# Kernel optimization log

Measured on AMD Instinct MI355X. Metric: run time of the kernel, lower is better.

## Reference

```python
import jax, jax.numpy as jnp
import numpy as np

INPUT_SIZE = 128
OUTPUT_SIZE = 200000
K = 4096
MOMENTUM = 0.5
BATCH = 128


def setup_inputs() -> dict:
    key = jax.random.key(0)
    k1, k2, k3, k4, k5, k6, k7, k8 = jax.random.split(key, 8)
    stdv = 1.0 / np.sqrt(INPUT_SIZE / 3.0)
    inp = {
        "l": jax.random.normal(k1, (BATCH, INPUT_SIZE), jnp.float32),
        "ab": jax.random.normal(k2, (BATCH, INPUT_SIZE), jnp.float32),
        "ori": jax.random.normal(k3, (BATCH, INPUT_SIZE), jnp.float32),
        "y": jax.random.randint(k4, (BATCH,), 0, OUTPUT_SIZE, jnp.int32),
        "idx": jax.random.randint(k5, (BATCH, K + 1), 0, OUTPUT_SIZE, jnp.int32),
        # memory banks ~ U(-stdv, stdv), as in the torch buffer init
        "memory_l": jax.random.uniform(k6, (OUTPUT_SIZE, INPUT_SIZE), jnp.float32, -stdv, stdv),
        "memory_ab": jax.random.uniform(k7, (OUTPUT_SIZE, INPUT_SIZE), jnp.float32, -stdv, stdv),
        "memory_ori": jax.random.uniform(k8, (OUTPUT_SIZE, INPUT_SIZE), jnp.float32, -stdv, stdv),
    }
    return inp


def reference(l, ab, ori, y, idx, memory_l, memory_ab, memory_ori):
    # Gather [B, K+1, D] slices from each memory bank (detached in original).
    w_l = jax.lax.stop_gradient(memory_l[idx])
    w_ab = jax.lax.stop_gradient(memory_ab[idx])
    w_ori = jax.lax.stop_gradient(memory_ori[idx])

    # bmm((B,K+1,D), (B,D,1)) -> (B,K+1); stack 6 score tensors -> (6,B,K+1)
    out_ab2l = jnp.einsum("bkd,bd->bk", w_l, ab)
    out_l2ab = jnp.einsum("bkd,bd->bk", w_ab, l)
    out_l2ori = jnp.einsum("bkd,bd->bk", w_ori, l)
    out_ori2l = jnp.einsum("bkd,bd->bk", w_l, ori)
    out_ori2ab = jnp.einsum("bkd,bd->bk", w_ab, ori)
    out_ab2ori = jnp.einsum("bkd,bd->bk", w_ori, ab)
    outs = jnp.stack([out_ab2l, out_l2ab, out_ori2l, out_l2ori, out_ab2ori, out_ori2ab])

    # Momentum scatter update of the memory banks (no_grad in original).
    def momentum_update(mem, feat):
        pos = mem[y] * MOMENTUM + feat * (1.0 - MOMENTUM)        # (B, D)
        norm = jnp.sqrt(jnp.sum(pos * pos, axis=1, keepdims=True))
        return mem.at[y].set(pos / norm)

    new_l = momentum_update(memory_l, l)
    new_ab = momentum_update(memory_ab, ab)
    new_ori = momentum_update(memory_ori, ori)
    return outs, new_l, new_ab, new_ori
```

## Files before the change

kernel.cpp:

```cpp
#include <hip/hip_runtime.h>

#define BATCH 128
#define DIM 128
#define KP1 4097
#define NOUT 200000
#define MEM_N (NOUT * DIM)

__global__ void momentum_rows(const float* __restrict__ l,
                              const float* __restrict__ ab,
                              const float* __restrict__ ori,
                              const int*   __restrict__ y,
                              const float* __restrict__ ml,
                              const float* __restrict__ mab,
                              const float* __restrict__ mo,
                              float* __restrict__ out_l,
                              float* __restrict__ out_ab,
                              float* __restrict__ out_o) {
    const int b  = blockIdx.x;
    const int yb = y[b];
    for (int b2 = b + 1; b2 < BATCH; ++b2)
        if (y[b2] == yb) return;

    const int t = threadIdx.x;
    const size_t mbase = (size_t)yb * DIM + t;
    const int    fbase = b * DIM + t;

    float p0 = ml [mbase] * 0.5f + l  [fbase] * 0.5f;
    float p1 = mab[mbase] * 0.5f + ab [fbase] * 0.5f;
    float p2 = mo [mbase] * 0.5f + ori[fbase] * 0.5f;

    float s0 = p0 * p0, s1 = p1 * p1, s2 = p2 * p2;
#pragma unroll
    for (int off = 32; off > 0; off >>= 1) {
        s0 += __shfl_down(s0, off, 64);
        s1 += __shfl_down(s1, off, 64);
        s2 += __shfl_down(s2, off, 64);
    }
    __shared__ float red[3][2];
    if ((t & 63) == 0) { red[0][t >> 6] = s0; red[1][t >> 6] = s1; red[2][t >> 6] = s2; }
    __syncthreads();
    const float i0 = 1.0f / sqrtf(red[0][0] + red[0][1]);
    const float i1 = 1.0f / sqrtf(red[1][0] + red[1][1]);
    const float i2 = 1.0f / sqrtf(red[2][0] + red[2][1]);

    out_l [mbase] = p0 * i0;
    out_ab[mbase] = p1 * i1;
    out_o [mbase] = p2 * i2;
}

__global__ __launch_bounds__(256) void bank_copy(const float4* __restrict__ ml,
                                                 const float4* __restrict__ mab,
                                                 const float4* __restrict__ mo,
                                                 float4* __restrict__ ol,
                                                 float4* __restrict__ oab,
                                                 float4* __restrict__ oo) {
    const int n = MEM_N / 4;
    const int stride = gridDim.x * blockDim.x;
    for (int i = blockIdx.x * blockDim.x + threadIdx.x; i < n; i += stride) {
        ol [i] = ml [i];
        oab[i] = mab[i];
        oo [i] = mo [i];
    }
}

__global__ __launch_bounds__(256) void scores_kernel(const float* __restrict__ l,
                                                     const float* __restrict__ ab,
                                                     const float* __restrict__ ori,
                                                     const int*   __restrict__ idx,
                                                     const float* __restrict__ ml,
                                                     const float* __restrict__ mab,
                                                     const float* __restrict__ mo,
                                                     float* __restrict__ out) {
    const int b    = blockIdx.y;
    const int t    = threadIdx.x;
    const int g    = t >> 4;
    const int lane = t & 15;
    const int k    = blockIdx.x * 16 + g;
    if (k >= KP1) return;

    const int row = idx[b * KP1 + k];

    const float4* rl4 = (const float4*)(ml  + (size_t)row * DIM);
    const float4* ra4 = (const float4*)(mab + (size_t)row * DIM);
    const float4* ro4 = (const float4*)(mo  + (size_t)row * DIM);

    float4 wl0 = rl4[lane], wl1 = rl4[lane + 16];
    float4 wa0 = ra4[lane], wa1 = ra4[lane + 16];
    float4 wo0 = ro4[lane], wo1 = ro4[lane + 16];

    const float4* fl4 = (const float4*)(l   + b * DIM);
    const float4* fa4 = (const float4*)(ab  + b * DIM);
    const float4* fo4 = (const float4*)(ori + b * DIM);
    float4 fl0 = fl4[lane], fl1 = fl4[lane + 16];
    float4 fa0 = fa4[lane], fa1 = fa4[lane + 16];
    float4 fo0 = fo4[lane], fo1 = fo4[lane + 16];

#define DOT8(w0, w1, f0, f1)                                                  \
    ((w0).x * (f0).x + (w0).y * (f0).y + (w0).z * (f0).z + (w0).w * (f0).w +  \
     (w1).x * (f1).x + (w1).y * (f1).y + (w1).z * (f1).z + (w1).w * (f1).w)

    float a0 = DOT8(wl0, wl1, fa0, fa1);
    float a1 = DOT8(wa0, wa1, fl0, fl1);
    float a2 = DOT8(wl0, wl1, fo0, fo1);
    float a3 = DOT8(wo0, wo1, fl0, fl1);
    float a4 = DOT8(wo0, wo1, fa0, fa1);
    float a5 = DOT8(wa0, wa1, fo0, fo1);
#undef DOT8

#pragma unroll
    for (int m = 8; m >= 1; m >>= 1) {
        a0 += __shfl_xor(a0, m, 16);
        a1 += __shfl_xor(a1, m, 16);
        a2 += __shfl_xor(a2, m, 16);
        a3 += __shfl_xor(a3, m, 16);
        a4 += __shfl_xor(a4, m, 16);
        a5 += __shfl_xor(a5, m, 16);
    }

    if (lane == 0) {
        const size_t plane = (size_t)BATCH * KP1;
        const size_t base  = (size_t)b * KP1 + k;
        out[base]             = a0;
        out[plane + base]     = a1;
        out[2 * plane + base] = a2;
        out[3 * plane + base] = a3;
        out[4 * plane + base] = a4;
        out[5 * plane + base] = a5;
    }
}

extern "C" void kernel_launch(void* const* d_in, const int* in_sizes, int n_in,
                              void* d_out, int out_size, void* d_ws, size_t ws_size,
                              hipStream_t stream) {
    const float* l   = (const float*)d_in[0];
    const float* ab  = (const float*)d_in[1];
    const float* ori = (const float*)d_in[2];
    const int*   y   = (const int*)d_in[3];
    const int*   idx = (const int*)d_in[4];
    const float* ml  = (const float*)d_in[5];
    const float* mab = (const float*)d_in[6];
    const float* mo  = (const float*)d_in[7];

    float* out        = (float*)d_out;
    float* out_scores = out;
    float* out_l  = out + (size_t)6 * BATCH * KP1;
    float* out_ab = out_l  + (size_t)MEM_N;
    float* out_o  = out_ab + (size_t)MEM_N;

    dim3 sgrid((KP1 + 15) / 16, BATCH);
    scores_kernel<<<sgrid, 256, 0, stream>>>(l, ab, ori, idx, ml, mab, mo, out_scores);

    bank_copy<<<2048, 256, 0, stream>>>((const float4*)ml, (const float4*)mab,
                                        (const float4*)mo,
                                        (float4*)out_l, (float4*)out_ab, (float4*)out_o);

    momentum_rows<<<BATCH, DIM, 0, stream>>>(l, ab, ori, y, ml, mab, mo,
                                             out_l, out_ab, out_o);
}
```

Measured before the change: 636.6 us.

## Fuse bank copy and score gather into one interleaved kernel with nontemporal copies

After: 624.0 us. 2.0% less time.

```diff
diff --git a/kernel.cpp b/kernel.cpp
--- a/kernel.cpp
+++ b/kernel.cpp
@@ -5,6 +5,14 @@
 #define KP1 4097
 #define NOUT 200000
 #define MEM_N (NOUT * DIM)
+
+#define NCOPY 2048
+#define KBLKS ((KP1 + 15) / 16)
+#define NSCORE (KBLKS * BATCH)
+#define NTOT (NCOPY + NSCORE)
+#define RILV 17
+
+typedef float fx4 __attribute__((ext_vector_type(4)));
 
 __global__ void momentum_rows(const float* __restrict__ l,
                               const float* __restrict__ ab,
@@ -48,34 +56,50 @@
     out_o [mbase] = p2 * i2;
 }
 
-__global__ __launch_bounds__(256) void bank_copy(const float4* __restrict__ ml,
-                                                 const float4* __restrict__ mab,
-                                                 const float4* __restrict__ mo,
-                                                 float4* __restrict__ ol,
-                                                 float4* __restrict__ oab,
-                                                 float4* __restrict__ oo) {
-    const int n = MEM_N / 4;
-    const int stride = gridDim.x * blockDim.x;
-    for (int i = blockIdx.x * blockDim.x + threadIdx.x; i < n; i += stride) {
-        ol [i] = ml [i];
-        oab[i] = mab[i];
-        oo [i] = mo [i];
+__global__ __launch_bounds__(256) void fused_kernel(const float* __restrict__ l,
+                                                    const float* __restrict__ ab,
+                                                    const float* __restrict__ ori,
+                                                    const int*   __restrict__ idx,
+                                                    const float* __restrict__ ml,
+                                                    const float* __restrict__ mab,
+                                                    const float* __restrict__ mo,
+                                                    float* __restrict__ out,
+                                                    float* __restrict__ out_l,
+                                                    float* __restrict__ out_ab,
+                                                    float* __restrict__ out_o) {
+    const int bid = blockIdx.x;
+    const int c   = bid / RILV;
+    const int r   = bid - c * RILV;
+
+    if (r == 0 && c < NCOPY) {
+        const fx4* ml4  = (const fx4*)ml;
+        const fx4* mab4 = (const fx4*)mab;
+        const fx4* mo4  = (const fx4*)mo;
+        fx4* ol4  = (fx4*)out_l;
+        fx4* oab4 = (fx4*)out_ab;
+        fx4* oo4  = (fx4*)out_o;
+        const int n = MEM_N / 4;
+        const int stride = NCOPY * 256;
+        for (int i = c * 256 + threadIdx.x; i < n; i += stride) {
+            fx4 a = __builtin_nontemporal_load(ml4 + i);
+            fx4 d = __builtin_nontemporal_load(mab4 + i);
+            fx4 e = __builtin_nontemporal_load(mo4 + i);
+            __builtin_nontemporal_store(a, ol4 + i);
+            __builtin_nontemporal_store(d, oab4 + i);
+            __builtin_nontemporal_store(e, oo4 + i);
+        }
+        return;
     }
-}
 
-__global__ __launch_bounds__(256) void scores_kernel(const float* __restrict__ l,
-                                                     const float* __restrict__ ab,
-                                                     const float* __restrict__ ori,
-                                                     const int*   __restrict__ idx,
-                                                     const float* __restrict__ ml,
-                                                     const float* __restrict__ mab,
-                                                     const float* __restrict__ mo,
-                                                     float* __restrict__ out) {
-    const int b    = blockIdx.y;
+    const int ncb = (r == 0) ? NCOPY : ((c + 1 < NCOPY) ? c + 1 : NCOPY);
+    const int sb  = bid - ncb;
+    const int b   = sb / KBLKS;
+    const int kb  = sb - b * KBLKS;
+
     const int t    = threadIdx.x;
     const int g    = t >> 4;
     const int lane = t & 15;
-    const int k    = blockIdx.x * 16 + g;
+    const int k    = kb * 16 + g;
     if (k >= KP1) return;
 
     const int row = idx[b * KP1 + k];
@@ -147,12 +171,8 @@
     float* out_ab = out_l  + (size_t)MEM_N;
     float* out_o  = out_ab + (size_t)MEM_N;
 
-    dim3 sgrid((KP1 + 15) / 16, BATCH);
-    scores_kernel<<<sgrid, 256, 0, stream>>>(l, ab, ori, idx, ml, mab, mo, out_scores);
-
-    bank_copy<<<2048, 256, 0, stream>>>((const float4*)ml, (const float4*)mab,
-                                        (const float4*)mo,
-                                        (float4*)out_l, (float4*)out_ab, (float4*)out_o);
+    fused_kernel<<<NTOT, 256, 0, stream>>>(l, ab, ori, idx, ml, mab, mo,
+                                           out_scores, out_l, out_ab, out_o);
 
     momentum_rows<<<BATCH, DIM, 0, stream>>>(l, ab, ori, y, ml, mab, mo,
                                              out_l, out_ab, out_o);
```
